# Performance work log

Measured on AMD Instinct MI355X. Metric: run time of the kernel, lower is better.

## Reference

```python
import jax, jax.numpy as jnp
import numpy as np

HIDDEN = 300
LN_EPS = 1e-5


def _pair_indices(L, K):
    # row-major (emo, cau) order matches torch cat/reshape in couple_generator
    i = np.arange(L)[:, None]
    j = np.arange(L)[None, :]
    mask = np.abs(j - i) <= K
    emo, cau = np.nonzero(mask)
    return emo.astype(np.int32), cau.astype(np.int32)


def setup_inputs() -> dict:
    key = jax.random.key(0)
    ks = jax.random.split(key, 10)
    B, L, D = 32, 128, HIDDEN
    K = 12
    pos_dim = 50
    inp = {
        "h_e": jax.random.normal(ks[0], (B, L, D), jnp.float32),
        "h_c": jax.random.normal(ks[1], (B, L, D), jnp.float32),
        "h_share": jax.random.normal(ks[2], (B, L, D), jnp.float32),
        "pos_emb": jax.random.normal(ks[3], (2 * K + 1, pos_dim), jnp.float32) * 0.1,
        "W_hid": jax.random.normal(ks[4], (D, 2 * D + pos_dim), jnp.float32) * 0.02,
        "b_hid": jnp.zeros((D,), jnp.float32),
        "ln_g": jnp.ones((D,), jnp.float32),
        "ln_b": jnp.zeros((D,), jnp.float32),
        "W_rel": jax.random.normal(ks[5], (1, D), jnp.float32) * 0.02,
        "b_rel": jnp.zeros((1,), jnp.float32),
        "K": K,
    }
    return inp


def reference(h_e, h_c, h_share, pos_emb, W_hid, b_hid, ln_g, ln_b, W_rel, b_rel, K):
    B, L, D = h_e.shape
    he = h_e + h_share
    hc = h_c + h_share
    emo, cau = _pair_indices(L, int(K))  # static index constants
    rel = (cau - emo).astype(np.float32)  # [n]
    rp = jnp.asarray(cau - emo + int(K), jnp.int32)  # shifted rel pos
    # gather-concat pair features: [B, n, 2D]
    couples = jnp.concatenate([he[:, emo, :], hc[:, cau, :]], axis=-1)
    # Gaussian kernel over relative positions: [n, n]
    rel_j = jnp.asarray(rel)
    kernel = jnp.exp(-jnp.square(rel_j[:, None] - rel_j[None, :]))
    # smooth position embeddings (batch-independent): [n, pos_dim]
    rel_pos_emb = kernel @ pos_emb[rp]
    pair = jnp.concatenate(
        [couples, jnp.broadcast_to(rel_pos_emb[None], (B,) + rel_pos_emb.shape)],
        axis=-1,
    )
    h = jnp.einsum("bnf,df->bnd", pair, W_hid) + b_hid
    mu = jnp.mean(h, axis=-1, keepdims=True)
    var = jnp.mean(jnp.square(h - mu), axis=-1, keepdims=True)
    h = (h - mu) * jax.lax.rsqrt(var + LN_EPS) * ln_g + ln_b
    h = jax.nn.elu(h)  # dropout is identity in eval mode
    out = jnp.einsum("bnd,od->bno", h, W_rel) + b_rel
    return out[..., 0]  # [B, n_couple]
```

## Files before the change

### kernel.cpp

```cpp
#include <hip/hip_runtime.h>
#include <hip/hip_bf16.h>
#include <math.h>

#define BB 32
#define LL 128
#define DD 300
#define PD 50
#define KW 12
#define NP 3044
#define FF 650
#define NR 25
#define KP 320
#define NPAD 320
#define MM 4096
#define LN_EPS 1e-5f

typedef __attribute__((ext_vector_type(8))) short short8;
typedef __attribute__((ext_vector_type(4))) float f32x4;
typedef __attribute__((ext_vector_type(4))) int i32x4;

__device__ __forceinline__ unsigned short f2b(float f) {
    union { float f; unsigned int u; } v; v.f = f;
    unsigned int u = v.u;
    unsigned int r = u + 0x7FFFu + ((u >> 16) & 1u);
    return (unsigned short)(r >> 16);
}

__device__ __forceinline__ int row_start(int i) {
    if (i <= 12) return i * 13 + (i * (i - 1)) / 2;
    if (i <= 116) return 222 + 25 * (i - 12);
    int s = i - 116;
    return 2822 + 24 * s - (s * (s - 1)) / 2;
}

#define PREP_W_BLOCKS 800

__global__ __launch_bounds__(256) void prep_kernel(
    const float* __restrict__ pos_emb, const float* __restrict__ W_hid,
    const float* __restrict__ b_hid, float* __restrict__ P,
    unsigned short* __restrict__ Wbf)
{
    const int tid = threadIdx.x;
    if (blockIdx.x < NR) {
        __shared__ float sm[PD];
        const int r = blockIdx.x;
        if (tid < PD) {
            float acc = 0.f;
            #pragma unroll
            for (int d = 0; d < NR; d++) {
                int ad = d - KW; if (ad < 0) ad = -ad;
                float cnt = (float)(LL - ad);
                float diff = (float)(r - d);
                acc += cnt * expf(-diff * diff) * pos_emb[d * PD + tid];
            }
            sm[tid] = acc;
        }
        __syncthreads();
        for (int dd = tid; dd < DD; dd += 256) {
            float a = b_hid[dd];
            const float* w = W_hid + dd * FF + 2 * DD;
            #pragma unroll
            for (int k = 0; k < PD; k++) a += sm[k] * w[k];
            P[r * DD + dd] = a;
        }
    } else {
        int idx = (blockIdx.x - NR) * 256 + tid;
        int z = idx / (NPAD * KP);
        int rem = idx - z * (NPAD * KP);
        int d = rem / KP;
        int k = rem - d * KP;
        unsigned short v = 0;
        if (d < DD && k < DD) v = f2b(W_hid[d * FF + z * DD + k]);
        Wbf[idx] = v;
    }
}

__global__ __launch_bounds__(256) void gemm_kernel(
    const float* __restrict__ h_e, const float* __restrict__ h_c,
    const float* __restrict__ h_share, const unsigned short* __restrict__ Wbf,
    float* __restrict__ E, float* __restrict__ Cc)
{
    __shared__ unsigned short Bs[160 * 40];

    const int z = blockIdx.z;
    const int m0 = blockIdx.x * 64;
    const int n0 = blockIdx.y * 160;
    const int tid = threadIdx.x;
    const int wid = tid >> 6;
    const int lane = tid & 63;
    const int nn = lane & 15;
    const int q  = lane >> 4;

    const int row = m0 + wid * 16 + nn;
    const float* xr = (z ? h_c : h_e) + (size_t)row * DD;
    const float* sr = h_share + (size_t)row * DD;
    const unsigned short* Wbase = Wbf + (size_t)(z * NPAD + n0) * KP;

    f32x4 acc[10];
    #pragma unroll
    for (int f = 0; f < 10; f++) acc[f] = (f32x4){0.f, 0.f, 0.f, 0.f};

    for (int k0 = 0; k0 < KP; k0 += 32) {
        for (int i = tid; i < 640; i += 256) {
            int n = i >> 2;
            int c = i & 3;
            i32x4 v = *(const i32x4*)&Wbase[n * KP + k0 + c * 8];
            *(i32x4*)&Bs[n * 40 + c * 8] = v;
        }
        __syncthreads();

        const int kb = k0 + q * 8;
        float a8[8];
        if (kb + 7 < DD) {
            float4 x0 = *(const float4*)&xr[kb];
            float4 x1 = *(const float4*)&xr[kb + 4];
            float4 s0 = *(const float4*)&sr[kb];
            float4 s1 = *(const float4*)&sr[kb + 4];
            a8[0] = x0.x + s0.x; a8[1] = x0.y + s0.y;
            a8[2] = x0.z + s0.z; a8[3] = x0.w + s0.w;
            a8[4] = x1.x + s1.x; a8[5] = x1.y + s1.y;
            a8[6] = x1.z + s1.z; a8[7] = x1.w + s1.w;
        } else {
            #pragma unroll
            for (int u = 0; u < 8; u++) {
                int k = kb + u;
                a8[u] = (k < DD) ? (xr[k] + sr[k]) : 0.f;
            }
        }
        short8 a;
        #pragma unroll
        for (int u = 0; u < 8; u++) a[u] = (short)f2b(a8[u]);

        #pragma unroll
        for (int f = 0; f < 10; f++) {
            short8 b = *(const short8*)&Bs[(f * 16 + nn) * 40 + q * 8];
            acc[f] = __builtin_amdgcn_mfma_f32_16x16x32_bf16(a, b, acc[f], 0, 0, 0);
        }
        __syncthreads();
    }

    float* O = z ? Cc : E;
    const int orow = m0 + wid * 16 + q * 4;
    #pragma unroll
    for (int f = 0; f < 10; f++) {
        int col = n0 + f * 16 + nn;
        if (col < DD) {
            #pragma unroll
            for (int r = 0; r < 4; r++)
                O[(size_t)(orow + r) * DD + col] = acc[f][r];
        }
    }
}

__global__ __launch_bounds__(256) void pair_kernel(
    const float* __restrict__ E, const float* __restrict__ Cc,
    const float* __restrict__ P, const float* __restrict__ ln_g,
    const float* __restrict__ ln_b, const float* __restrict__ W_rel,
    const float* __restrict__ b_rel, float* __restrict__ out)
{
    const int wid = threadIdx.x >> 6;
    const int lane = threadIdx.x & 63;
    const int slot = blockIdx.x;
    const int b = slot >> 7;
    const int i = slot & 127;

    const float* e_row = E + (size_t)(b * LL + i) * DD;

    float e[5], g[5], gb[5], wr[5];
    #pragma unroll
    for (int t = 0; t < 5; t++) {
        int d = lane + 64 * t;
        if (d < DD) {
            e[t]  = e_row[d];
            g[t]  = ln_g[d];
            gb[t] = ln_b[d];
            wr[t] = W_rel[d];
        } else {
            e[t] = 0.f; g[t] = 0.f; gb[t] = 0.f; wr[t] = 0.f;
        }
    }
    const float brel = b_rel[0];

    int jlo = i - KW; if (jlo < 0) jlo = 0;
    int jhi = i + KW; if (jhi > LL - 1) jhi = LL - 1;
    const int base = b * NP + row_start(i);

    for (int j = jlo + wid; j <= jhi; j += 4) {
        const float* c_row = Cc + (size_t)(b * LL + j) * DD;
        const float* p_row = P + (j - i + KW) * DD;

        float h[5];
        float s = 0.f, ss = 0.f;
        #pragma unroll
        for (int t = 0; t < 5; t++) {
            int d = lane + 64 * t;
            h[t] = 0.f;
            if (d < DD) {
                h[t] = e[t] + c_row[d] + p_row[d];
                s += h[t];
                ss += h[t] * h[t];
            }
        }
        #pragma unroll
        for (int m = 1; m < 64; m <<= 1) {
            s  += __shfl_xor(s, m, 64);
            ss += __shfl_xor(ss, m, 64);
        }
        const float mean = s * (1.f / (float)DD);
        float var = ss * (1.f / (float)DD) - mean * mean;
        if (var < 0.f) var = 0.f;
        const float rstd = rsqrtf(var + LN_EPS);

        float acc = 0.f;
        #pragma unroll
        for (int t = 0; t < 5; t++) {
            int d = lane + 64 * t;
            if (d < DD) {
                float y = (h[t] - mean) * rstd * g[t] + gb[t];
                float el = y > 0.f ? y : (__expf(y) - 1.f);
                acc += el * wr[t];
            }
        }
        #pragma unroll
        for (int m = 1; m < 64; m <<= 1) acc += __shfl_xor(acc, m, 64);

        if (lane == 0) out[base + (j - jlo)] = acc + brel;
    }
}

extern "C" void kernel_launch(void* const* d_in, const int* in_sizes, int n_in,
                              void* d_out, int out_size, void* d_ws, size_t ws_size,
                              hipStream_t stream) {
    const float* h_e     = (const float*)d_in[0];
    const float* h_c     = (const float*)d_in[1];
    const float* h_share = (const float*)d_in[2];
    const float* pos_emb = (const float*)d_in[3];
    const float* W_hid   = (const float*)d_in[4];
    const float* b_hid   = (const float*)d_in[5];
    const float* ln_g    = (const float*)d_in[6];
    const float* ln_b    = (const float*)d_in[7];
    const float* W_rel   = (const float*)d_in[8];
    const float* b_rel   = (const float*)d_in[9];

    float* out = (float*)d_out;

    float* ws = (float*)d_ws;
    float* E   = ws;
    float* C   = E + (size_t)MM * DD;
    float* P   = C + (size_t)MM * DD;
    unsigned short* Wbf = (unsigned short*)(P + NR * DD);

    prep_kernel<<<dim3(NR + PREP_W_BLOCKS), dim3(256), 0, stream>>>(
        pos_emb, W_hid, b_hid, P, Wbf);

    gemm_kernel<<<dim3(MM / 64, 2, 2), dim3(256), 0, stream>>>(
        h_e, h_c, h_share, Wbf, E, C);

    pair_kernel<<<dim3(BB * LL), dim3(256), 0, stream>>>(
        E, C, P, ln_g, ln_b, W_rel, b_rel, out);
}
```

Baseline: 131.2 us.

## Fuse weight conversion into GEMM, double-buffer B, precompute row sums for LayerNorm

Drops the separate bf16 weight-conversion pass and converts W_hid to bf16 inside the GEMM with packed cvt instructions. The GEMM now uses 512-thread blocks with LDS double buffering and register prefetch, and it is merged into one launch with the position-projection blocks. The GEMM also writes per-row partial sums of E, C and P, so the pair kernel gets the LayerNorm mean without a second wave reduction. The pair kernel moves to 5 waves per block and reorders blocks to spread the batch. This removes one launch and one global round trip of the weights, in exchange for redoing the conversion in every GEMM block and computing the mean from separately summed partials.

Measured after the change: 128.1 us, median of 2. 1.02x faster.

```diff
diff --git a/kernel.cpp b/kernel.cpp
--- a/kernel.cpp
+++ b/kernel.cpp
@@ -1,5 +1,4 @@
 #include <hip/hip_runtime.h>
-#include <hip/hip_bf16.h>
 #include <math.h>
 
 #define BB 32
@@ -11,7 +10,6 @@
 #define FF 650
 #define NR 25
 #define KP 320
-#define NPAD 320
 #define MM 4096
 #define LN_EPS 1e-5f
 
@@ -19,11 +17,14 @@
 typedef __attribute__((ext_vector_type(4))) float f32x4;
 typedef __attribute__((ext_vector_type(4))) int i32x4;
 
-__device__ __forceinline__ unsigned short f2b(float f) {
-    union { float f; unsigned int u; } v; v.f = f;
-    unsigned int u = v.u;
-    unsigned int r = u + 0x7FFFu + ((u >> 16) & 1u);
-    return (unsigned short)(r >> 16);
+__device__ __forceinline__ unsigned int cvtpk(float lo, float hi) {
+    unsigned int r;
+    asm("v_cvt_pk_bf16_f32 %0, %1, %2" : "=v"(r) : "v"(lo), "v"(hi));
+    return r;
+}
+
+__device__ __forceinline__ short8 as_short8(i32x4 v) {
+    union { i32x4 i; short8 s; } u; u.i = v; return u.s;
 }
 
 __device__ __forceinline__ int row_start(int i) {
@@ -33,138 +34,225 @@
     return 2822 + 24 * s - (s * (s - 1)) / 2;
 }
 
-#define PREP_W_BLOCKS 800
-
-__global__ __launch_bounds__(256) void prep_kernel(
-    const float* __restrict__ pos_emb, const float* __restrict__ W_hid,
-    const float* __restrict__ b_hid, float* __restrict__ P,
-    unsigned short* __restrict__ Wbf)
+struct B8 { float f[8]; };
+
+__global__ __launch_bounds__(512) void fused_kernel(
+    const float* __restrict__ h_e, const float* __restrict__ h_c,
+    const float* __restrict__ h_share, const float* __restrict__ pos_emb,
+    const float* __restrict__ W_hid, const float* __restrict__ b_hid,
+    float* __restrict__ E, float* __restrict__ Cc, float* __restrict__ P,
+    float* __restrict__ SEp, float* __restrict__ SP)
 {
     const int tid = threadIdx.x;
+
+    __shared__ unsigned short Bs[2][160 * 40];
+
     if (blockIdx.x < NR) {
         __shared__ float sm[PD];
+        __shared__ float wsum[8];
         const int r = blockIdx.x;
         if (tid < PD) {
             float acc = 0.f;
             #pragma unroll
-            for (int d = 0; d < NR; d++) {
-                int ad = d - KW; if (ad < 0) ad = -ad;
+            for (int d2 = 0; d2 < NR; d2++) {
+                int ad = d2 - KW; if (ad < 0) ad = -ad;
                 float cnt = (float)(LL - ad);
-                float diff = (float)(r - d);
-                acc += cnt * expf(-diff * diff) * pos_emb[d * PD + tid];
+                float diff = (float)(r - d2);
+                acc += cnt * expf(-diff * diff) * pos_emb[d2 * PD + tid];
             }
             sm[tid] = acc;
         }
         __syncthreads();
-        for (int dd = tid; dd < DD; dd += 256) {
-            float a = b_hid[dd];
-            const float* w = W_hid + dd * FF + 2 * DD;
+        float mine = 0.f;
+        if (tid < DD) {
+            float a = b_hid[tid];
+            const float* w = W_hid + (size_t)tid * FF + 2 * DD;
             #pragma unroll
             for (int k = 0; k < PD; k++) a += sm[k] * w[k];
-            P[r * DD + dd] = a;
-        }
-    } else {
-        int idx = (blockIdx.x - NR) * 256 + tid;
-        int z = idx / (NPAD * KP);
-        int rem = idx - z * (NPAD * KP);
-        int d = rem / KP;
-        int k = rem - d * KP;
-        unsigned short v = 0;
-        if (d < DD && k < DD) v = f2b(W_hid[d * FF + z * DD + k]);
-        Wbf[idx] = v;
-    }
-}
-
-__global__ __launch_bounds__(256) void gemm_kernel(
-    const float* __restrict__ h_e, const float* __restrict__ h_c,
-    const float* __restrict__ h_share, const unsigned short* __restrict__ Wbf,
-    float* __restrict__ E, float* __restrict__ Cc)
-{
-    __shared__ unsigned short Bs[160 * 40];
-
-    const int z = blockIdx.z;
-    const int m0 = blockIdx.x * 64;
-    const int n0 = blockIdx.y * 160;
-    const int tid = threadIdx.x;
-    const int wid = tid >> 6;
+            P[r * DD + tid] = a;
+            mine = a;
+        }
+        #pragma unroll
+        for (int m = 1; m < 64; m <<= 1) mine += __shfl_xor(mine, m, 64);
+        if ((tid & 63) == 0) wsum[tid >> 6] = mine;
+        __syncthreads();
+        if (tid == 0) {
+            float s = 0.f;
+            #pragma unroll
+            for (int w = 0; w < 8; w++) s += wsum[w];
+            SP[r] = s;
+        }
+        return;
+    }
+
+    const int gb = blockIdx.x - NR;
+    const int sg = (gb & 7) * 32 + (gb >> 3);
+    const int m0 = (sg & 63) * 64;
+    const int y  = (sg >> 6) & 1;
+    const int z  = sg >> 7;
+    const int n0 = y * 160;
+
+    const int wid  = tid >> 6;
     const int lane = tid & 63;
+    const int wm = wid & 3;
+    const int wn = wid >> 1 >> 1;
     const int nn = lane & 15;
     const int q  = lane >> 4;
 
-    const int row = m0 + wid * 16 + nn;
+    const int row = m0 + wm * 16 + nn;
     const float* xr = (z ? h_c : h_e) + (size_t)row * DD;
     const float* sr = h_share + (size_t)row * DD;
-    const unsigned short* Wbase = Wbf + (size_t)(z * NPAD + n0) * KP;
-
-    f32x4 acc[10];
-    #pragma unroll
-    for (int f = 0; f < 10; f++) acc[f] = (f32x4){0.f, 0.f, 0.f, 0.f};
-
-    for (int k0 = 0; k0 < KP; k0 += 32) {
-        for (int i = tid; i < 640; i += 256) {
-            int n = i >> 2;
-            int c = i & 3;
-            i32x4 v = *(const i32x4*)&Wbase[n * KP + k0 + c * 8];
-            *(i32x4*)&Bs[n * 40 + c * 8] = v;
-        }
-        __syncthreads();
-
+    const float* Wsrc = W_hid + z * DD;
+
+    const int n_a = tid >> 2,        c_a = tid & 3;
+    const int d_a = n0 + n_a;
+    const int n_b = (tid + 512) >> 2;
+    const int d_b = n0 + n_b;
+    const bool has_b = (tid < 128);
+
+    B8 ra, rb;
+    float4 ax0, ax1, as0, as1;
+
+    auto loadB = [&](int k0) {
+        const float* pa = Wsrc + (size_t)d_a * FF + k0 + c_a * 8;
+        float2 u0 = *(const float2*)(pa);
+        float2 u1 = *(const float2*)(pa + 2);
+        float2 u2 = *(const float2*)(pa + 4);
+        float2 u3 = *(const float2*)(pa + 6);
+        ra.f[0] = u0.x; ra.f[1] = u0.y; ra.f[2] = u1.x; ra.f[3] = u1.y;
+        ra.f[4] = u2.x; ra.f[5] = u2.y; ra.f[6] = u3.x; ra.f[7] = u3.y;
+        if (has_b) {
+            if (d_b < DD) {
+                const float* pb = Wsrc + (size_t)d_b * FF + k0 + c_a * 8;
+                float2 v0 = *(const float2*)(pb);
+                float2 v1 = *(const float2*)(pb + 2);
+                float2 v2 = *(const float2*)(pb + 4);
+                float2 v3 = *(const float2*)(pb + 6);
+                rb.f[0] = v0.x; rb.f[1] = v0.y; rb.f[2] = v1.x; rb.f[3] = v1.y;
+                rb.f[4] = v2.x; rb.f[5] = v2.y; rb.f[6] = v3.x; rb.f[7] = v3.y;
+            } else {
+                #pragma unroll
+                for (int u = 0; u < 8; u++) rb.f[u] = 0.f;
+            }
+        }
+    };
+
+    auto writeB = [&](int buf) {
+        i32x4 w;
+        w[0] = cvtpk(ra.f[0], ra.f[1]); w[1] = cvtpk(ra.f[2], ra.f[3]);
+        w[2] = cvtpk(ra.f[4], ra.f[5]); w[3] = cvtpk(ra.f[6], ra.f[7]);
+        *(i32x4*)&Bs[buf][n_a * 40 + c_a * 8] = w;
+        if (has_b) {
+            i32x4 v;
+            v[0] = cvtpk(rb.f[0], rb.f[1]); v[1] = cvtpk(rb.f[2], rb.f[3]);
+            v[2] = cvtpk(rb.f[4], rb.f[5]); v[3] = cvtpk(rb.f[6], rb.f[7]);
+            *(i32x4*)&Bs[buf][n_b * 40 + c_a * 8] = v;
+        }
+    };
+
+    auto loadA = [&](int k0) {
         const int kb = k0 + q * 8;
-        float a8[8];
         if (kb + 7 < DD) {
-            float4 x0 = *(const float4*)&xr[kb];
-            float4 x1 = *(const float4*)&xr[kb + 4];
-            float4 s0 = *(const float4*)&sr[kb];
-            float4 s1 = *(const float4*)&sr[kb + 4];
-            a8[0] = x0.x + s0.x; a8[1] = x0.y + s0.y;
-            a8[2] = x0.z + s0.z; a8[3] = x0.w + s0.w;
-            a8[4] = x1.x + s1.x; a8[5] = x1.y + s1.y;
-            a8[6] = x1.z + s1.z; a8[7] = x1.w + s1.w;
+            ax0 = *(const float4*)&xr[kb];
+            ax1 = *(const float4*)&xr[kb + 4];
+            as0 = *(const float4*)&sr[kb];
+            as1 = *(const float4*)&sr[kb + 4];
         } else {
-            #pragma unroll
-            for (int u = 0; u < 8; u++) {
-                int k = kb + u;
-                a8[u] = (k < DD) ? (xr[k] + sr[k]) : 0.f;
-            }
-        }
-        short8 a;
-        #pragma unroll
-        for (int u = 0; u < 8; u++) a[u] = (short)f2b(a8[u]);
-
-        #pragma unroll
-        for (int f = 0; f < 10; f++) {
-            short8 b = *(const short8*)&Bs[(f * 16 + nn) * 40 + q * 8];
+            float t[8], u[8];
+            #pragma unroll
+            for (int uu = 0; uu < 8; uu++) {
+                int k = kb + uu;
+                t[uu] = (k < DD) ? xr[k] : 0.f;
+                u[uu] = (k < DD) ? sr[k] : 0.f;
+            }
+            ax0 = make_float4(t[0], t[1], t[2], t[3]);
+            ax1 = make_float4(t[4], t[5], t[6], t[7]);
+            as0 = make_float4(u[0], u[1], u[2], u[3]);
+            as1 = make_float4(u[4], u[5], u[6], u[7]);
+        }
+    };
+
+    f32x4 acc[5];
+    #pragma unroll
+    for (int f = 0; f < 5; f++) acc[f] = (f32x4){0.f, 0.f, 0.f, 0.f};
+
+    loadB(0);
+    loadA(0);
+    writeB(0);
+    __syncthreads();
+
+    #pragma unroll
+    for (int k0i = 0; k0i < 10; k0i++) {
+        const int cb = k0i & 1;
+        const bool more = (k0i < 9);
+        const int kn = (k0i + 1) * 32;
+
+        if (more) loadB(kn);
+
+        i32x4 af;
+        af[0] = cvtpk(ax0.x + as0.x, ax0.y + as0.y);
+        af[1] = cvtpk(ax0.z + as0.z, ax0.w + as0.w);
+        af[2] = cvtpk(ax1.x + as1.x, ax1.y + as1.y);
+        af[3] = cvtpk(ax1.z + as1.z, ax1.w + as1.w);
+        short8 a = as_short8(af);
+
+        if (more) loadA(kn);
+
+        #pragma unroll
+        for (int f = 0; f < 5; f++) {
+            short8 b = *(const short8*)&Bs[cb][(wn * 80 + f * 16 + nn) * 40 + q * 8];
             acc[f] = __builtin_amdgcn_mfma_f32_16x16x32_bf16(a, b, acc[f], 0, 0, 0);
         }
-        __syncthreads();
+
+        if (more) {
+            writeB(cb ^ 1);
+            __syncthreads();
+        }
+    }
+
+    const int orow = m0 + wm * 16 + q * 4;
+    float rs[4];
+    #pragma unroll
+    for (int r2 = 0; r2 < 4; r2++) {
+        float v = 0.f;
+        #pragma unroll
+        for (int f = 0; f < 5; f++) v += acc[f][r2];
+        #pragma unroll
+        for (int m = 1; m < 16; m <<= 1) v += __shfl_xor(v, m, 64);
+        rs[r2] = v;
+    }
+    if (nn == 0) {
+        float* slot = SEp + (size_t)(((z * 2 + y) * 2 + wn)) * MM;
+        #pragma unroll
+        for (int r2 = 0; r2 < 4; r2++) slot[orow + r2] = rs[r2];
     }
 
     float* O = z ? Cc : E;
-    const int orow = m0 + wid * 16 + q * 4;
-    #pragma unroll
-    for (int f = 0; f < 10; f++) {
-        int col = n0 + f * 16 + nn;
+    #pragma unroll
+    for (int f = 0; f < 5; f++) {
+        int col = n0 + wn * 80 + f * 16 + nn;
         if (col < DD) {
             #pragma unroll
-            for (int r = 0; r < 4; r++)
-                O[(size_t)(orow + r) * DD + col] = acc[f][r];
-        }
-    }
-}
-
-__global__ __launch_bounds__(256) void pair_kernel(
+            for (int r2 = 0; r2 < 4; r2++)
+                O[(size_t)(orow + r2) * DD + col] = acc[f][r2];
+        }
+    }
+}
+
+__global__ __launch_bounds__(320) void pair_kernel(
     const float* __restrict__ E, const float* __restrict__ Cc,
-    const float* __restrict__ P, const float* __restrict__ ln_g,
+    const float* __restrict__ P, const float* __restrict__ SEp,
+    const float* __restrict__ SP, const float* __restrict__ ln_g,
     const float* __restrict__ ln_b, const float* __restrict__ W_rel,
     const float* __restrict__ b_rel, float* __restrict__ out)
 {
     const int wid = threadIdx.x >> 6;
     const int lane = threadIdx.x & 63;
-    const int slot = blockIdx.x;
+    const int slot = (blockIdx.x & 7) * 512 + (blockIdx.x >> 3);
     const int b = slot >> 7;
     const int i = slot & 127;
 
-    const float* e_row = E + (size_t)(b * LL + i) * DD;
+    const float* e_row = E + (size_t)slot * DD;
 
     float e[5], g[5], gb[5], wr[5];
     #pragma unroll
@@ -180,34 +268,39 @@
         }
     }
     const float brel = b_rel[0];
+    const float SEi = SEp[slot] + SEp[MM + slot] + SEp[2 * MM + slot] + SEp[3 * MM + slot];
+    const float* SC = SEp + 4 * MM;
 
     int jlo = i - KW; if (jlo < 0) jlo = 0;
     int jhi = i + KW; if (jhi > LL - 1) jhi = LL - 1;
     const int base = b * NP + row_start(i);
-
-    for (int j = jlo + wid; j <= jhi; j += 4) {
-        const float* c_row = Cc + (size_t)(b * LL + j) * DD;
-        const float* p_row = P + (j - i + KW) * DD;
+    const float inv = 1.f / (float)DD;
+
+    for (int j = jlo + wid; j <= jhi; j += 5) {
+        const int bj = b * LL + j;
+        const int r = j - i + KW;
+        const float* c_row = Cc + (size_t)bj * DD;
+        const float* p_row = P + r * DD;
+
+        const float sumh = SEi + SC[bj] + SC[MM + bj] + SC[2 * MM + bj]
+                         + SC[3 * MM + bj] + SP[r];
 
         float h[5];
-        float s = 0.f, ss = 0.f;
+        float ss = 0.f;
         #pragma unroll
         for (int t = 0; t < 5; t++) {
             int d = lane + 64 * t;
             h[t] = 0.f;
             if (d < DD) {
                 h[t] = e[t] + c_row[d] + p_row[d];
-                s += h[t];
                 ss += h[t] * h[t];
             }
         }
         #pragma unroll
-        for (int m = 1; m < 64; m <<= 1) {
-            s  += __shfl_xor(s, m, 64);
-            ss += __shfl_xor(ss, m, 64);
-        }
-        const float mean = s * (1.f / (float)DD);
-        float var = ss * (1.f / (float)DD) - mean * mean;
+        for (int m = 1; m < 64; m <<= 1) ss += __shfl_xor(ss, m, 64);
+
+        const float mean = sumh * inv;
+        float var = ss * inv - mean * mean;
         if (var < 0.f) var = 0.f;
         const float rstd = rsqrtf(var + LN_EPS);
 
@@ -216,8 +309,8 @@
         for (int t = 0; t < 5; t++) {
             int d = lane + 64 * t;
             if (d < DD) {
-                float y = (h[t] - mean) * rstd * g[t] + gb[t];
-                float el = y > 0.f ? y : (__expf(y) - 1.f);
+                float yv = (h[t] - mean) * rstd * g[t] + gb[t];
+                float el = yv > 0.f ? yv : (__expf(yv) - 1.f);
                 acc += el * wr[t];
             }
         }
@@ -244,18 +337,16 @@
 
     float* out = (float*)d_out;
 
-    float* ws = (float*)d_ws;
+    float* ws  = (float*)d_ws;
     float* E   = ws;
     float* C   = E + (size_t)MM * DD;
     float* P   = C + (size_t)MM * DD;
-    unsigned short* Wbf = (unsigned short*)(P + NR * DD);
-
-    prep_kernel<<<dim3(NR + PREP_W_BLOCKS), dim3(256), 0, stream>>>(
-        pos_emb, W_hid, b_hid, P, Wbf);
-
-    gemm_kernel<<<dim3(MM / 64, 2, 2), dim3(256), 0, stream>>>(
-        h_e, h_c, h_share, Wbf, E, C);
-
-    pair_kernel<<<dim3(BB * LL), dim3(256), 0, stream>>>(
-        E, C, P, ln_g, ln_b, W_rel, b_rel, out);
-}
+    float* SEp = P + NR * DD;
+    float* SP  = SEp + 8 * MM;
+
+    fused_kernel<<<dim3(NR + 256), dim3(512), 0, stream>>>(
+        h_e, h_c, h_share, pos_emb, W_hid, b_hid, E, C, P, SEp, SP);
+
+    pair_kernel<<<dim3(BB * LL), dim3(320), 0, stream>>>(
+        E, C, P, SEp, SP, ln_g, ln_b, W_rel, b_rel, out);
+}
```
